# Kernel optimization log

Measured on AMD Instinct MI355X. Metric: run time of the kernel, lower is better.

Reference implementation:

```python
import jax, jax.numpy as jnp
import numpy as np

H_OUT = 7
W_OUT = 7
SCALE = 1.0 / 16.0


def setup_inputs() -> dict:
    key = jax.random.key(0)
    k1, k2, k3, k4 = jax.random.split(key, 4)
    N, C, h, w = 2, 512, 50, 50      # VGG16 conv5 features of an 800x800 image (stride 16)
    R = 128                          # rois per minibatch
    img = 800.0
    x = jax.random.normal(k1, (N, C, h, w), dtype=jnp.float32)
    batch = jax.random.randint(k2, (R,), 0, N).astype(jnp.float32)
    pt1 = jax.random.uniform(k3, (R, 2), minval=0.0, maxval=img - 32.0)   # (y1, x1)
    sz = jax.random.uniform(k4, (R, 2), minval=32.0, maxval=400.0)
    pt2 = jnp.minimum(pt1 + sz, img - 1.0)                                # (y2, x2)
    rois = jnp.concatenate(
        [batch[:, None], pt1[:, 0:1], pt1[:, 1:2], pt2[:, 0:1], pt2[:, 1:2]], axis=1
    )
    return {"x": x, "rois": rois}


def roi_pool(x, rois, H=H_OUT, W=W_OUT, scale=SCALE):
    # Faithful to the source: each ROI is zero-padded up to multiples of (H, W),
    # tiled into non-overlapping HxW windows, and the output is the elementwise
    # max across windows (padding zeros participate in the max).
    N, C, h, w = x.shape
    R = rois.shape[0]
    bidx = rois[:, 0].astype(jnp.int32)
    bb = jnp.round(rois[:, 1:5] * scale).astype(jnp.int32)   # (y1, x1, y2, x2)
    y1, x1 = bb[:, 0], bb[:, 1]
    y2 = jnp.minimum(bb[:, 2], h - 1)   # torch slicing x[..., y1:y2+1] clips at h
    x2 = jnp.minimum(bb[:, 3], w - 1)

    ys = jnp.arange(h)
    xs = jnp.arange(w)
    in_y = (ys[None, :] >= y1[:, None]) & (ys[None, :] <= y2[:, None])   # [R, h]
    in_x = (xs[None, :] >= x1[:, None]) & (xs[None, :] <= x2[:, None])   # [R, w]
    a = jnp.mod(ys[None, :] - y1[:, None], H)   # within-window row   [R, h]
    b = jnp.mod(xs[None, :] - x1[:, None], W)   # within-window col   [R, w]

    valid = in_y[:, :, None] & in_x[:, None, :]                 # [R, h, w]
    bin_id = a[:, :, None] * W + b[:, None, :]                  # [R, h, w]
    roi_off = jnp.arange(R)[:, None, None] * (H * W)
    dump = R * H * W                                            # bin for pixels outside any ROI
    seg = jnp.where(valid, roi_off + bin_id, dump).reshape(-1)  # [R*h*w]

    vals = x[bidx]                                              # [R, C, h, w] gather per ROI
    vals = vals.transpose(0, 2, 3, 1).reshape(-1, C)            # [R*h*w, C]
    seg_max = jax.ops.segment_max(vals, seg, num_segments=R * H * W + 1)[: R * H * W]
    seg_max = seg_max.reshape(R, H, W, C).transpose(0, 3, 1, 2)  # [R, C, H, W]

    # Zero padding contributes to the max at bin (a, b) iff the ROI extent is not
    # an exact multiple of H (resp. W) and a >= ft_h % H (resp. b >= ft_w % W).
    ft_h = y2 - y1 + 1
    ft_w = x2 - x1 + 1
    rem_h = jnp.mod(ft_h, H)
    rem_w = jnp.mod(ft_w, W)
    pad_h = (rem_h[:, None] != 0) & (jnp.arange(H)[None, :] >= rem_h[:, None])  # [R, H]
    pad_w = (rem_w[:, None] != 0) & (jnp.arange(W)[None, :] >= rem_w[:, None])  # [R, W]
    zero_inc = pad_h[:, None, :, None] | pad_w[:, None, None, :]                # [R, 1, H, W]
    return jnp.where(zero_inc, jnp.maximum(seg_max, 0), seg_max).astype(x.dtype)


def reference(x, rois):
    return roi_pool(x, rois)
```

## Files before the change

### kernel.cpp

```cpp
#include <hip/hip_runtime.h>
#include <math.h>


#define CH 512
#define IH 50
#define IW 50
#define NEG_INF (-__builtin_inff())

__global__ __launch_bounds__(256) void roipool_kernel(
    const float* __restrict__ x, const float* __restrict__ rois,
    float* __restrict__ out) {
  const int r    = blockIdx.y;
  const int wave = threadIdx.x >> 6;
  const int lane = threadIdx.x & 63;
  const int half = lane >> 5;
  const int dx   = lane & 31;

  const float* rr = rois + r * 5;
  const int b  = (int)rr[0];
  const int y1 = (int)rintf(rr[1] * 0.0625f);
  const int x1 = (int)rintf(rr[2] * 0.0625f);
  const int y2 = min((int)rintf(rr[3] * 0.0625f), IH - 1);
  const int x2 = min((int)rintf(rr[4] * 0.0625f), IW - 1);
  const int fth  = y2 - y1 + 1;
  const int ftw  = x2 - x1 + 1;
  const int remh = fth % 7;
  const int remw = ftw % 7;

  const int c = (blockIdx.x * 4 + wave) * 2 + half;
  const float* base = x + ((size_t)(b * CH + c) * IH + y1) * IW + x1 + dx;
  const bool colok = dx < ftw;

  float acc[7];
#pragma unroll
  for (int i = 0; i < 7; ++i) acc[i] = NEG_INF;

  const int nsr = (fth + 6) / 7;
  for (int s = 0; s < nsr; ++s) {
    const float* rowb = base + (s * 7) * IW;
#pragma unroll
    for (int i = 0; i < 7; ++i) {
      const int dy = s * 7 + i;
      float v = NEG_INF;
      if ((dy < fth) & colok) v = rowb[i * IW];
      acc[i] = fmaxf(acc[i], v);
    }
  }

#pragma unroll
  for (int i = 0; i < 7; ++i) {
    float a = acc[i];
    a = fmaxf(a, __shfl_down(a, 7, 64));
    a = fmaxf(a, __shfl_down(a, 14, 64));
    acc[i] = a;
  }

  if (dx < 7) {
    const int j = dx;
    const bool padc = (remw != 0) && (j >= remw);
    float* o = out + (size_t)(r * CH + c) * 49 + j;
#pragma unroll
    for (int i = 0; i < 7; ++i) {
      float v = acc[i];
      const bool padr = (remh != 0) && (i >= remh);
      if (padr | padc) v = fmaxf(v, 0.0f);
      o[i * 7] = v;
    }
  }
}

extern "C" void kernel_launch(void* const* d_in, const int* in_sizes, int n_in,
                              void* d_out, int out_size, void* d_ws, size_t ws_size,
                              hipStream_t stream) {
  const float* x    = (const float*)d_in[0];
  const float* rois = (const float*)d_in[1];
  float* out        = (float*)d_out;
  const int R = in_sizes[1] / 5;

  dim3 grid(64, R);
  dim3 block(256);
  roipool_kernel<<<grid, block, 0, stream>>>(x, rois, out);
}
```

Measured before the change: 73.33 us.

## Process two channels per half-wave, split full and tail row strips

Each half-wave now handles two channels, so the grid is halved and twice as many independent loads are in flight per thread. ROI coordinates are made wave-uniform through readfirstlane so they live in scalar registers. The main loop covers only full 7-row strips with no per-row bound check, and a separate tail handles the remainder rows. Column indices are clamped so loads stay in range without predicating them, with masking applied afterward. The trade-off is fewer blocks and waves for latency hiding, plus higher register use.

```diff
diff --git a/kernel.cpp b/kernel.cpp
--- a/kernel.cpp
+++ b/kernel.cpp
@@ -17,54 +17,81 @@
   const int dx   = lane & 31;
 
   const float* rr = rois + r * 5;
-  const int b  = (int)rr[0];
-  const int y1 = (int)rintf(rr[1] * 0.0625f);
-  const int x1 = (int)rintf(rr[2] * 0.0625f);
-  const int y2 = min((int)rintf(rr[3] * 0.0625f), IH - 1);
-  const int x2 = min((int)rintf(rr[4] * 0.0625f), IW - 1);
+  const int b  = __builtin_amdgcn_readfirstlane((int)rr[0]);
+  const int y1 = __builtin_amdgcn_readfirstlane((int)rintf(rr[1] * 0.0625f));
+  const int x1 = __builtin_amdgcn_readfirstlane((int)rintf(rr[2] * 0.0625f));
+  const int y2 = __builtin_amdgcn_readfirstlane(min((int)rintf(rr[3] * 0.0625f), IH - 1));
+  const int x2 = __builtin_amdgcn_readfirstlane(min((int)rintf(rr[4] * 0.0625f), IW - 1));
   const int fth  = y2 - y1 + 1;
   const int ftw  = x2 - x1 + 1;
   const int remh = fth % 7;
   const int remw = ftw % 7;
+  const int full = fth / 7;
 
-  const int c = (blockIdx.x * 4 + wave) * 2 + half;
-  const float* base = x + ((size_t)(b * CH + c) * IH + y1) * IW + x1 + dx;
+  const int cbase = (blockIdx.x * 4 + wave) * 4 + half * 2;
+  const int cx    = min(dx, ftw - 1);
   const bool colok = dx < ftw;
 
-  float acc[7];
+  const float* b0 = x + ((size_t)(b * CH + cbase) * IH + y1) * IW + x1 + cx;
+  const float* b1 = b0 + (size_t)IH * IW;
+
+  float acc0[7], acc1[7];
 #pragma unroll
-  for (int i = 0; i < 7; ++i) acc[i] = NEG_INF;
+  for (int i = 0; i < 7; ++i) { acc0[i] = NEG_INF; acc1[i] = NEG_INF; }
 
-  const int nsr = (fth + 6) / 7;
-  for (int s = 0; s < nsr; ++s) {
-    const float* rowb = base + (s * 7) * IW;
+  for (int s = 0; s < full; ++s) {
+    const float* r0 = b0 + s * 7 * IW;
+    const float* r1 = b1 + s * 7 * IW;
 #pragma unroll
     for (int i = 0; i < 7; ++i) {
-      const int dy = s * 7 + i;
-      float v = NEG_INF;
-      if ((dy < fth) & colok) v = rowb[i * IW];
-      acc[i] = fmaxf(acc[i], v);
+      float v0 = r0[i * IW];
+      float v1 = r1[i * IW];
+      v0 = colok ? v0 : NEG_INF;
+      v1 = colok ? v1 : NEG_INF;
+      acc0[i] = fmaxf(acc0[i], v0);
+      acc1[i] = fmaxf(acc1[i], v1);
+    }
+  }
+
+  {
+    const float* t0 = b0 + full * 7 * IW;
+    const float* t1 = b1 + full * 7 * IW;
+#pragma unroll
+    for (int i = 0; i < 7; ++i) {
+      if (i < remh) {
+        float v0 = t0[i * IW];
+        float v1 = t1[i * IW];
+        v0 = colok ? v0 : NEG_INF;
+        v1 = colok ? v1 : NEG_INF;
+        acc0[i] = fmaxf(acc0[i], v0);
+        acc1[i] = fmaxf(acc1[i], v1);
+      }
     }
   }
 
 #pragma unroll
   for (int i = 0; i < 7; ++i) {
-    float a = acc[i];
-    a = fmaxf(a, __shfl_down(a, 7, 64));
-    a = fmaxf(a, __shfl_down(a, 14, 64));
-    acc[i] = a;
+    float a0 = acc0[i], a1 = acc1[i];
+    a0 = fmaxf(a0, __shfl_down(a0, 7, 64));
+    a1 = fmaxf(a1, __shfl_down(a1, 7, 64));
+    a0 = fmaxf(a0, __shfl_down(a0, 14, 64));
+    a1 = fmaxf(a1, __shfl_down(a1, 14, 64));
+    acc0[i] = a0;
+    acc1[i] = a1;
   }
 
   if (dx < 7) {
     const int j = dx;
     const bool padc = (remw != 0) && (j >= remw);
-    float* o = out + (size_t)(r * CH + c) * 49 + j;
+    float* o0 = out + (size_t)(r * CH + cbase) * 49 + j;
+    float* o1 = o0 + 49;
 #pragma unroll
     for (int i = 0; i < 7; ++i) {
-      float v = acc[i];
+      float v0 = acc0[i], v1 = acc1[i];
       const bool padr = (remh != 0) && (i >= remh);
-      if (padr | padc) v = fmaxf(v, 0.0f);
-      o[i * 7] = v;
+      if (padr | padc) { v0 = fmaxf(v0, 0.0f); v1 = fmaxf(v1, 0.0f); }
+      o0[i * 7] = v0;
+      o1[i * 7] = v1;
     }
   }
 }
@@ -77,7 +104,7 @@
   float* out        = (float*)d_out;
   const int R = in_sizes[1] / 5;
 
-  dim3 grid(64, R);
+  dim3 grid(32, R);
   dim3 block(256);
   roipool_kernel<<<grid, block, 0, stream>>>(x, rois, out);
 }
```

After: 71.05 us. 3.1% less time.

## Process four channels per half-wave and remap out-of-range columns to in-window duplicates

Applied to the files above, without the earlier changes.

Each half-wave now handles four channels instead of one, so the grid shrinks fourfold and more independent loads are in flight per thread. Lanes past the ROI width are redirected to earlier columns congruent mod 7, which keeps the max unchanged and removes per-load masking when the width is at least 7. Row bounds are split into full 7-row strips plus a remainder, and ROI scalars are made wave-uniform with readfirstlane. In exchange, register use rises to 28 accumulators per thread and there are fewer blocks to spread across CUs.

```diff
diff --git a/kernel.cpp b/kernel.cpp
--- a/kernel.cpp
+++ b/kernel.cpp
@@ -5,7 +5,41 @@
 #define CH 512
 #define IH 50
 #define IW 50
+#define PLANE (IH * IW)
 #define NEG_INF (-__builtin_inff())
+
+template <bool MASK>
+__device__ __forceinline__ void run_rows(const float* __restrict__ b0,
+                                         int full, int remh, bool colok,
+                                         float (&acc)[4][7]) {
+  const float* __restrict__ bp[4] = {b0, b0 + PLANE, b0 + 2 * PLANE, b0 + 3 * PLANE};
+
+  for (int s = 0; s < full; ++s) {
+    const int off = s * 7 * IW;
+#pragma unroll
+    for (int i = 0; i < 7; ++i) {
+#pragma unroll
+      for (int p = 0; p < 4; ++p) {
+        float v = bp[p][off + i * IW];
+        if (MASK) v = colok ? v : NEG_INF;
+        acc[p][i] = fmaxf(acc[p][i], v);
+      }
+    }
+  }
+
+  const int toff = full * 7 * IW;
+#pragma unroll
+  for (int i = 0; i < 7; ++i) {
+    if (i < remh) {
+#pragma unroll
+      for (int p = 0; p < 4; ++p) {
+        float v = bp[p][toff + i * IW];
+        if (MASK) v = colok ? v : NEG_INF;
+        acc[p][i] = fmaxf(acc[p][i], v);
+      }
+    }
+  }
+}
 
 __global__ __launch_bounds__(256) void roipool_kernel(
     const float* __restrict__ x, const float* __restrict__ rois,
@@ -17,54 +51,64 @@
   const int dx   = lane & 31;
 
   const float* rr = rois + r * 5;
-  const int b  = (int)rr[0];
-  const int y1 = (int)rintf(rr[1] * 0.0625f);
-  const int x1 = (int)rintf(rr[2] * 0.0625f);
-  const int y2 = min((int)rintf(rr[3] * 0.0625f), IH - 1);
-  const int x2 = min((int)rintf(rr[4] * 0.0625f), IW - 1);
+  const int b  = __builtin_amdgcn_readfirstlane((int)rr[0]);
+  const int y1 = __builtin_amdgcn_readfirstlane((int)rintf(rr[1] * 0.0625f));
+  const int x1 = __builtin_amdgcn_readfirstlane((int)rintf(rr[2] * 0.0625f));
+  const int y2 = __builtin_amdgcn_readfirstlane(min((int)rintf(rr[3] * 0.0625f), IH - 1));
+  const int x2 = __builtin_amdgcn_readfirstlane(min((int)rintf(rr[4] * 0.0625f), IW - 1));
   const int fth  = y2 - y1 + 1;
   const int ftw  = x2 - x1 + 1;
   const int remh = fth % 7;
   const int remw = ftw % 7;
+  const int full = fth / 7;
 
-  const int c = (blockIdx.x * 4 + wave) * 2 + half;
-  const float* base = x + ((size_t)(b * CH + c) * IH + y1) * IW + x1 + dx;
+  const int cbase = (blockIdx.x * 4 + wave) * 8 + half * 4;
+
+  int cx = dx;
+  cx = (cx >= ftw) ? cx - 7 : cx;
+  cx = (cx >= ftw) ? cx - 7 : cx;
+  cx = (cx >= ftw) ? cx - 7 : cx;
+  cx = (cx >= ftw) ? cx - 7 : cx;
+  const bool ftw_small = ftw < 7;
   const bool colok = dx < ftw;
+  const int  cxs   = min(dx, ftw - 1);
 
-  float acc[7];
+  const float* b0 = x + (size_t)(b * CH + cbase) * PLANE + (y1 * IW + x1)
+                      + (ftw_small ? cxs : cx);
+
+  float acc[4][7];
 #pragma unroll
-  for (int i = 0; i < 7; ++i) acc[i] = NEG_INF;
+  for (int p = 0; p < 4; ++p)
+#pragma unroll
+    for (int i = 0; i < 7; ++i) acc[p][i] = NEG_INF;
 
-  const int nsr = (fth + 6) / 7;
-  for (int s = 0; s < nsr; ++s) {
-    const float* rowb = base + (s * 7) * IW;
+  if (!ftw_small) run_rows<false>(b0, full, remh, true,  acc);
+  else            run_rows<true >(b0, full, remh, colok, acc);
+
+#pragma unroll
+  for (int p = 0; p < 4; ++p) {
 #pragma unroll
     for (int i = 0; i < 7; ++i) {
-      const int dy = s * 7 + i;
-      float v = NEG_INF;
-      if ((dy < fth) & colok) v = rowb[i * IW];
-      acc[i] = fmaxf(acc[i], v);
+      float a = acc[p][i];
+      a = fmaxf(a, __shfl_down(a, 7, 64));
+      a = fmaxf(a, __shfl_down(a, 14, 64));
+      acc[p][i] = a;
     }
-  }
-
-#pragma unroll
-  for (int i = 0; i < 7; ++i) {
-    float a = acc[i];
-    a = fmaxf(a, __shfl_down(a, 7, 64));
-    a = fmaxf(a, __shfl_down(a, 14, 64));
-    acc[i] = a;
   }
 
   if (dx < 7) {
     const int j = dx;
     const bool padc = (remw != 0) && (j >= remw);
-    float* o = out + (size_t)(r * CH + c) * 49 + j;
+    float* o = out + (size_t)(r * CH + cbase) * 49 + j;
 #pragma unroll
-    for (int i = 0; i < 7; ++i) {
-      float v = acc[i];
-      const bool padr = (remh != 0) && (i >= remh);
-      if (padr | padc) v = fmaxf(v, 0.0f);
-      o[i * 7] = v;
+    for (int p = 0; p < 4; ++p) {
+#pragma unroll
+      for (int i = 0; i < 7; ++i) {
+        float v = acc[p][i];
+        const bool padr = (remh != 0) && (i >= remh);
+        if (padr | padc) v = fmaxf(v, 0.0f);
+        o[p * 49 + i * 7] = v;
+      }
     }
   }
 }
@@ -77,7 +121,7 @@
   float* out        = (float*)d_out;
   const int R = in_sizes[1] / 5;
 
-  dim3 grid(64, R);
+  dim3 grid(16, R);
   dim3 block(256);
   roipool_kernel<<<grid, block, 0, stream>>>(x, rois, out);
 }
```

Result: slower. 76.75 us (+4.7%).
